# Kernel optimization log

Hardware: AMD Instinct MI355X
Metric: run time of the kernel (lower is better)

## Reference

```python
import jax, jax.numpy as jnp
import numpy as np

# Model dims (match init_kwargs)
E = 16            # real experts
Z = 16            # zero experts (identity)
TOP_K = 4
H = 1024          # hidden_size
I = 512           # intermediate_size per expert
T = 4096          # tokens
ROUTED_SCALING = 1.0


def setup_inputs() -> dict:
    key = jax.random.key(0)
    ks = jax.random.split(key, 6)
    s_h = 1.0 / np.sqrt(H)
    s_i = 1.0 / np.sqrt(I)
    return {
        "hidden_states": jax.random.normal(ks[0], (T, H), jnp.float32),
        # router over E + Z total slots (real experts + zero experts)
        "router_weight": jax.random.normal(ks[1], (E + Z, H), jnp.float32) * s_h,
        "e_score_bias": jax.random.normal(ks[2], (E + Z,), jnp.float32) * 0.01,
        # SwiGLU expert weights
        "w_gate": jax.random.normal(ks[3], (E, H, I), jnp.float32) * s_h,
        "w_up": jax.random.normal(ks[4], (E, H, I), jnp.float32) * s_h,
        "w_down": jax.random.normal(ks[5], (E, I, H), jnp.float32) * s_i,
    }


def reference(hidden_states, router_weight, e_score_bias, w_gate, w_up, w_down):
    x = hidden_states  # [T, H]
    # --- Router (float32, router_dtype == 'float32') ---
    logits = jnp.einsum("th,eh->te", x.astype(jnp.float32), router_weight)  # [T, E+Z]
    scores = jax.nn.softmax(logits, axis=-1)
    # top-k selected on bias-corrected scores; weights taken from raw scores,
    # renormalize=False
    _, topk_ids = jax.lax.top_k(scores + e_score_bias[None, :], TOP_K)  # [T, k]
    topk_w = jnp.take_along_axis(scores, topk_ids, axis=-1)             # [T, k]
    # --- Dispatch/combine weights over all E+Z slots ---
    onehot = jax.nn.one_hot(topk_ids, E + Z, dtype=jnp.float32)  # [T, k, E+Z]
    combine = jnp.einsum("tk,tks->ts", topk_w, onehot)           # [T, E+Z]
    cw_real = combine[:, :E].astype(x.dtype)      # [T, E] routed-expert weights
    zero_w = combine[:, E:].sum(-1).astype(x.dtype)  # [T] identity weight sum
    # --- Grouped-expert SwiGLU (dense dispatch reference) ---
    g = jnp.einsum("th,ehi->eti", x, w_gate)   # [E, T, I]
    u = jnp.einsum("th,ehi->eti", x, w_up)     # [E, T, I]
    act = jax.nn.silu(g) * u
    eout = jnp.einsum("eti,eih->eth", act, w_down)  # [E, T, H]
    routed = jnp.einsum("eth,te->th", eout, cw_real)  # [T, H]
    # zero experts: identity contribution (zero_expert_type == 'identity')
    out = routed * ROUTED_SCALING + zero_w[:, None] * x
    return out
```

## Files before the change

kernel.cpp:

```cpp
#include <hip/hip_runtime.h>
#include <stdint.h>

#define T_TOK 4096
#define Hd    1024
#define Id    512
#define NE    16
#define NSLOT 32
#define TOPK  4
#define CAPR  (T_TOK*TOPK)
#define MAXTILES 144

typedef __bf16 bf16x8 __attribute__((ext_vector_type(8)));
typedef float  floatx4 __attribute__((ext_vector_type(4)));

#define WAIT_VM(n) asm volatile("s_waitcnt vmcnt(" #n ")" ::: "memory")

static __device__ __forceinline__ void wg_barrier(){
  asm volatile("" ::: "memory");
  __builtin_amdgcn_s_barrier();
  asm volatile("" ::: "memory");
}

static __device__ __forceinline__ unsigned short f2bf(float f){
  unsigned int u = __float_as_uint(f);
  u = u + 0x7fffu + ((u >> 16) & 1u);
  return (unsigned short)(u >> 16);
}

static __device__ __forceinline__ void load_lds16(const void* g, void* l){
  __builtin_amdgcn_global_load_lds((const __attribute__((address_space(1))) void*)g,
                                   (__attribute__((address_space(3))) void*)l, 16, 0, 0);
}

__global__ __launch_bounds__(256) void cvt_x_kernel(const float* __restrict__ x,
                                                    unsigned short* __restrict__ xb){
  int i = blockIdx.x * 256 + threadIdx.x;
  float4 v = ((const float4*)x)[i];
  ushort4 o;
  o.x = f2bf(v.x); o.y = f2bf(v.y); o.z = f2bf(v.z); o.w = f2bf(v.w);
  ((ushort4*)xb)[i] = o;
}

__global__ __launch_bounds__(256) void transpose_cvt_kernel(
    const float* __restrict__ src, unsigned short* __restrict__ dst, int R, int C){
  __shared__ float tile[64][65];
  const int e = blockIdx.z;
  const int c0 = blockIdx.x * 64;
  const int r0 = blockIdx.y * 64;
  const float* s = src + (size_t)e * R * C;
  unsigned short* d = dst + (size_t)e * R * C;
  const int lr = threadIdx.x >> 4;
  const int lc = (threadIdx.x & 15) * 4;
  #pragma unroll
  for (int p = 0; p < 4; ++p){
    int r = p*16 + lr;
    float4 v = *(const float4*)(s + (size_t)(r0 + r)*C + c0 + lc);
    tile[r][lc+0] = v.x; tile[r][lc+1] = v.y; tile[r][lc+2] = v.z; tile[r][lc+3] = v.w;
  }
  __syncthreads();
  #pragma unroll
  for (int p = 0; p < 4; ++p){
    int c = p*16 + lr;
    ushort4 o;
    o.x = f2bf(tile[lc+0][c]); o.y = f2bf(tile[lc+1][c]);
    o.z = f2bf(tile[lc+2][c]); o.w = f2bf(tile[lc+3][c]);
    *(ushort4*)(d + (size_t)(c0 + c)*R + r0 + lc) = o;
  }
}

__global__ __launch_bounds__(256) void logits_kernel(const float* __restrict__ x,
    const float* __restrict__ rw, float* __restrict__ logits){
  __shared__ float srw[NSLOT][260];
  const int kc = blockIdx.y * 256;
  const int tid = threadIdx.x;
  #pragma unroll
  for (int p = 0; p < 8; ++p){
    int idx = tid + p*256;
    int s = idx >> 6;
    int c = (idx & 63) << 2;
    float4 v = *(const float4*)(rw + (size_t)s*Hd + kc + c);
    *(float4*)&srw[s][c] = v;
  }
  __syncthreads();
  const int tg = tid >> 3;
  const int sg = tid & 7;
  const int t0 = blockIdx.x * 128 + tg * 4;
  const int s0 = sg * 4;
  float acc[4][4] = {};
  for (int k = 0; k < 256; k += 4){
    float4 r0 = *(const float4*)&srw[s0+0][k];
    float4 r1 = *(const float4*)&srw[s0+1][k];
    float4 r2 = *(const float4*)&srw[s0+2][k];
    float4 r3 = *(const float4*)&srw[s0+3][k];
    #pragma unroll
    for (int tt = 0; tt < 4; ++tt){
      float4 xv = *(const float4*)(x + (size_t)(t0+tt)*Hd + kc + k);
      acc[tt][0] += xv.x*r0.x + xv.y*r0.y + xv.z*r0.z + xv.w*r0.w;
      acc[tt][1] += xv.x*r1.x + xv.y*r1.y + xv.z*r1.z + xv.w*r1.w;
      acc[tt][2] += xv.x*r2.x + xv.y*r2.y + xv.z*r2.z + xv.w*r2.w;
      acc[tt][3] += xv.x*r3.x + xv.y*r3.y + xv.z*r3.z + xv.w*r3.w;
    }
  }
  #pragma unroll
  for (int tt = 0; tt < 4; ++tt)
    #pragma unroll
    for (int s = 0; s < 4; ++s)
      atomicAdd(&logits[(size_t)(t0+tt)*NSLOT + s0 + s], acc[tt][s]);
}

__global__ __launch_bounds__(256) void topk_kernel(
    const float* __restrict__ logits, const float* __restrict__ bias,
    int* __restrict__ counts, int* __restrict__ tkid, float* __restrict__ tkw,
    float* __restrict__ zero_w){
  int t = blockIdx.x * 256 + threadIdx.x;
  float sc[32], bsc[32];
  #pragma unroll
  for (int i = 0; i < 32; i += 4){
    float4 v = *(const float4*)(logits + (size_t)t*NSLOT + i);
    sc[i] = v.x; sc[i+1] = v.y; sc[i+2] = v.z; sc[i+3] = v.w;
  }
  float mx = sc[0];
  #pragma unroll
  for (int i = 1; i < 32; ++i) mx = fmaxf(mx, sc[i]);
  float sum = 0.f;
  #pragma unroll
  for (int i = 0; i < 32; ++i){ sc[i] = __expf(sc[i]-mx); sum += sc[i]; }
  float inv = 1.f / sum;
  #pragma unroll
  for (int i = 0; i < 32; ++i){ sc[i] *= inv; bsc[i] = sc[i] + bias[i]; }
  unsigned int chosen = 0;
  float zw = 0.f;
  #pragma unroll
  for (int k = 0; k < TOPK; ++k){
    float bv = -1e30f, bw = 0.f; int best = 0;
    #pragma unroll
    for (int i = 0; i < 32; ++i){
      float v = ((chosen >> i) & 1u) ? -1e30f : bsc[i];
      if (v > bv){ bv = v; best = i; bw = sc[i]; }
    }
    chosen |= (1u << best);
    tkid[t*TOPK + k] = best;
    tkw[t*TOPK + k]  = bw;
    if (best < NE) atomicAdd(&counts[best], 1);
    else zw += bw;
  }
  zero_w[t] = zw;
}

__global__ void offsets_kernel(const int* __restrict__ counts,
                               int* __restrict__ offsets, int* __restrict__ cursors,
                               int* __restrict__ tilelist, int* __restrict__ ntiles){
  if (threadIdx.x == 0){
    int acc = 0;
    for (int e = 0; e < NE; ++e){ offsets[e] = acc; acc += counts[e]; }
    offsets[NE] = acc;
    int n = 0;
    for (int e = 0; e < NE; ++e){
      int ne = counts[e];
      for (int m = 0; m*128 < ne; ++m) tilelist[n++] = (e << 16) | m;
    }
    ntiles[0] = n;
  }
  if (threadIdx.x < NE) cursors[threadIdx.x] = 0;
}

__global__ __launch_bounds__(256) void build_kernel(
    const int* __restrict__ tkid, const float* __restrict__ tkw,
    const int* __restrict__ offsets, int* __restrict__ cursors,
    int* __restrict__ rowmap, float* __restrict__ roww){
  int i = blockIdx.x * 256 + threadIdx.x;
  int id = tkid[i];
  if (id < NE){
    int pos = atomicAdd(&cursors[id], 1);
    int row = offsets[id] + pos;
    rowmap[row] = i >> 2;
    roww[row]   = tkw[i];
  }
}

__global__ __launch_bounds__(256) void outinit_kernel(const float* __restrict__ x,
    const float* __restrict__ zw, float* __restrict__ out){
  int i = blockIdx.x * 256 + threadIdx.x;
  float s = zw[i >> 8];
  float4 v = ((const float4*)x)[i];
  float4 o; o.x = v.x*s; o.y = v.y*s; o.z = v.z*s; o.w = v.w*s;
  ((float4*)out)[i] = o;
}

__global__ __launch_bounds__(256, 2) void gateup_kernel(
    const unsigned short* __restrict__ xb,
    const unsigned short* __restrict__ wgb,
    const unsigned short* __restrict__ wub,
    const int* __restrict__ offsets,
    const int* __restrict__ rowmap,
    const float* __restrict__ roww,
    const int* __restrict__ tilelist,
    const int* __restrict__ ntiles,
    unsigned short* __restrict__ act){
  const int b = blockIdx.x;
  const int tile = b >> 2;
  if (tile >= ntiles[0]) return;
  const int packed = tilelist[tile];
  const int e  = packed >> 16;
  const int m0 = (packed & 0xffff) * 128;
  const int n0 = (b & 3) * 128;
  const int off = offsets[e];
  const int ne  = offsets[e+1] - off;

  __shared__ unsigned short sA [2][128*32];
  __shared__ unsigned short sBg[2][128*32];
  __shared__ unsigned short sBu[2][128*32];
  __shared__ int sT[128];

  const int tid  = threadIdx.x;
  const int lane = tid & 63;
  const int wid  = tid >> 6;

  if (tid < 128){
    int r = m0 + tid;
    sT[tid] = rowmap[off + ((r < ne) ? r : 0)];
  }
  __syncthreads();

  const int r_in = lane >> 2;
  const int seg  = lane & 3;
  const int rt0  = wid*32 + r_in;
  const int rt1  = rt0 + 16;
  const size_t wbase = (size_t)e * Id * Hd;

  const unsigned short* pA0 = xb + (size_t)sT[rt0]*Hd + seg*8;
  const unsigned short* pA1 = xb + (size_t)sT[rt1]*Hd + seg*8;
  const unsigned short* pG0 = wgb + wbase + (size_t)(n0+rt0)*Hd + seg*8;
  const unsigned short* pG1 = wgb + wbase + (size_t)(n0+rt1)*Hd + seg*8;
  const unsigned short* pU0 = wub + wbase + (size_t)(n0+rt0)*Hd + seg*8;
  const unsigned short* pU1 = wub + wbase + (size_t)(n0+rt1)*Hd + seg*8;
  const int dA0 = wid*1024;
  const int dA1 = wid*1024 + 512;

  floatx4 accg[4][4], accu[4][4];
  #pragma unroll
  for (int i = 0; i < 4; ++i)
    #pragma unroll
    for (int j = 0; j < 4; ++j){
      floatx4 z = {0.f,0.f,0.f,0.f};
      accg[i][j] = z; accu[i][j] = z;
    }

  const int wm = (wid & 1) * 64;
  const int wn = (wid >> 1) * 64;
  const int fm = lane & 15;
  const int fq = lane >> 4;

  load_lds16(pA0, &sA[0][dA0]);  load_lds16(pA1, &sA[0][dA1]);
  load_lds16(pG0, &sBg[0][dA0]); load_lds16(pG1, &sBg[0][dA1]);
  load_lds16(pU0, &sBu[0][dA0]); load_lds16(pU1, &sBu[0][dA1]);

  #pragma unroll 2
  for (int kit = 0; kit < 32; ++kit){
    const int cur = kit & 1;
    if (kit < 31){
      const int nk = (kit+1)*32;
      const int nb = 1 - cur;
      load_lds16(pA0 + nk, &sA[nb][dA0]);  load_lds16(pA1 + nk, &sA[nb][dA1]);
      load_lds16(pG0 + nk, &sBg[nb][dA0]); load_lds16(pG1 + nk, &sBg[nb][dA1]);
      load_lds16(pU0 + nk, &sBu[nb][dA0]); load_lds16(pU1 + nk, &sBu[nb][dA1]);
      WAIT_VM(6);
    } else {
      WAIT_VM(0);
    }
    wg_barrier();
    bf16x8 av[4], bgv[4], buv[4];
    #pragma unroll
    for (int i = 0; i < 4; ++i)
      av[i] = *(const bf16x8*)(&sA[cur][(wm + i*16 + fm)*32 + fq*8]);
    #pragma unroll
    for (int j = 0; j < 4; ++j){
      bgv[j] = *(const bf16x8*)(&sBg[cur][(wn + j*16 + fm)*32 + fq*8]);
      buv[j] = *(const bf16x8*)(&sBu[cur][(wn + j*16 + fm)*32 + fq*8]);
    }
    #pragma unroll
    for (int i = 0; i < 4; ++i)
      #pragma unroll
      for (int j = 0; j < 4; ++j){
        accg[i][j] = __builtin_amdgcn_mfma_f32_16x16x32_bf16(av[i], bgv[j], accg[i][j], 0, 0, 0);
        accu[i][j] = __builtin_amdgcn_mfma_f32_16x16x32_bf16(av[i], buv[j], accu[i][j], 0, 0, 0);
      }
    wg_barrier();
  }

  #pragma unroll
  for (int i = 0; i < 4; ++i){
    #pragma unroll
    for (int r = 0; r < 4; ++r){
      int row = wm + i*16 + fq*4 + r;
      if (m0 + row < ne){
        float w = roww[off + m0 + row];
        size_t rb = (size_t)(off + m0 + row) * Id + n0;
        #pragma unroll
        for (int j = 0; j < 4; ++j){
          float g = accg[i][j][r];
          float u = accu[i][j][r];
          float a = (g / (1.f + __expf(-g))) * u * w;
          act[rb + wn + j*16 + fm] = f2bf(a);
        }
      }
    }
  }
}

__global__ __launch_bounds__(256, 2) void down_kernel(
    const unsigned short* __restrict__ act,
    const unsigned short* __restrict__ wdb,
    const int* __restrict__ offsets,
    const int* __restrict__ rowmap,
    const int* __restrict__ tilelist,
    const int* __restrict__ ntiles,
    float* __restrict__ out){
  const int b = blockIdx.x;
  const int tile = b >> 3;
  if (tile >= ntiles[0]) return;
  const int packed = tilelist[tile];
  const int e  = packed >> 16;
  const int m0 = (packed & 0xffff) * 128;
  const int n0 = (b & 7) * 128;
  const int off = offsets[e];
  const int ne  = offsets[e+1] - off;

  __shared__ unsigned short sA[2][128*32];
  __shared__ unsigned short sB[2][128*32];
  __shared__ int sT[128];

  const int tid  = threadIdx.x;
  const int lane = tid & 63;
  const int wid  = tid >> 6;
  if (tid < 128){
    int r = m0 + tid;
    sT[tid] = (r < ne) ? rowmap[off + r] : 0;
  }

  const int r_in = lane >> 2, seg = lane & 3;
  const int rt0 = wid*32 + r_in;
  const int rt1 = rt0 + 16;
  const int gr0 = off + ((m0 + rt0 < ne) ? (m0 + rt0) : 0);
  const int gr1 = off + ((m0 + rt1 < ne) ? (m0 + rt1) : 0);
  const size_t wbase = (size_t)e * Hd * Id;
  const unsigned short* pA0 = act + (size_t)gr0*Id + seg*8;
  const unsigned short* pA1 = act + (size_t)gr1*Id + seg*8;
  const unsigned short* pB0 = wdb + wbase + (size_t)(n0+rt0)*Id + seg*8;
  const unsigned short* pB1 = wdb + wbase + (size_t)(n0+rt1)*Id + seg*8;
  const int dA0 = wid*1024, dA1 = wid*1024 + 512;

  floatx4 acc[4][4];
  #pragma unroll
  for (int i = 0; i < 4; ++i)
    #pragma unroll
    for (int j = 0; j < 4; ++j){ floatx4 z = {0.f,0.f,0.f,0.f}; acc[i][j] = z; }

  const int wm = (wid & 1) * 64, wn = (wid >> 1) * 64;
  const int fm = lane & 15, fq = lane >> 4;

  load_lds16(pA0, &sA[0][dA0]); load_lds16(pA1, &sA[0][dA1]);
  load_lds16(pB0, &sB[0][dA0]); load_lds16(pB1, &sB[0][dA1]);

  #pragma unroll 2
  for (int kit = 0; kit < 16; ++kit){
    const int cur = kit & 1;
    if (kit < 15){
      const int nk = (kit+1)*32;
      const int nb = 1 - cur;
      load_lds16(pA0 + nk, &sA[nb][dA0]); load_lds16(pA1 + nk, &sA[nb][dA1]);
      load_lds16(pB0 + nk, &sB[nb][dA0]); load_lds16(pB1 + nk, &sB[nb][dA1]);
      WAIT_VM(4);
    } else {
      WAIT_VM(0);
    }
    wg_barrier();
    bf16x8 av[4], bv[4];
    #pragma unroll
    for (int i = 0; i < 4; ++i) av[i] = *(const bf16x8*)(&sA[cur][(wm + i*16 + fm)*32 + fq*8]);
    #pragma unroll
    for (int j = 0; j < 4; ++j) bv[j] = *(const bf16x8*)(&sB[cur][(wn + j*16 + fm)*32 + fq*8]);
    #pragma unroll
    for (int i = 0; i < 4; ++i)
      #pragma unroll
      for (int j = 0; j < 4; ++j)
        acc[i][j] = __builtin_amdgcn_mfma_f32_16x16x32_bf16(av[i], bv[j], acc[i][j], 0, 0, 0);
    wg_barrier();
  }

  #pragma unroll
  for (int i = 0; i < 4; ++i){
    #pragma unroll
    for (int r = 0; r < 4; ++r){
      int row = wm + i*16 + fq*4 + r;
      if (m0 + row < ne){
        int t = sT[row];
        #pragma unroll
        for (int j = 0; j < 4; ++j)
          atomicAdd(&out[(size_t)t*Hd + n0 + wn + j*16 + fm], acc[i][j][r]);
      }
    }
  }
}

extern "C" void kernel_launch(void* const* d_in, const int* in_sizes, int n_in,
                              void* d_out, int out_size, void* d_ws, size_t ws_size,
                              hipStream_t stream){
  (void)in_sizes; (void)n_in; (void)out_size; (void)ws_size;
  const float* x    = (const float*)d_in[0];
  const float* rw   = (const float*)d_in[1];
  const float* bias = (const float*)d_in[2];
  const float* wg   = (const float*)d_in[3];
  const float* wu   = (const float*)d_in[4];
  const float* wd   = (const float*)d_in[5];
  float* out = (float*)d_out;

  char* ws = (char*)d_ws;
  const size_t WSZ = (size_t)NE * Id * Hd * 2;
  unsigned short* wgb = (unsigned short*)(ws);
  unsigned short* wub = (unsigned short*)(ws + WSZ);
  unsigned short* wdb = (unsigned short*)(ws + 2*WSZ);
  unsigned short* xb  = (unsigned short*)(ws + 3*WSZ);
  unsigned short* act = (unsigned short*)(ws + 3*WSZ + (size_t)T_TOK*Hd*2);
  char* misc = ws + 3*WSZ + (size_t)T_TOK*Hd*2 + (size_t)CAPR*Id*2;

  const size_t LOGB = (size_t)T_TOK * NSLOT * 4;
  float* logits = (float*)misc;
  int*   counts  = (int*)(misc + LOGB);
  int*   cursors = counts + 16;
  int*   offsets = cursors + 16;
  char* p2 = misc + LOGB + 256;
  int*   tkid   = (int*)p2;                         p2 += (size_t)T_TOK*TOPK*4;
  float* tkw    = (float*)p2;                       p2 += (size_t)T_TOK*TOPK*4;
  float* zerow  = (float*)p2;                       p2 += (size_t)T_TOK*4;
  int*   rowmap = (int*)p2;                         p2 += (size_t)CAPR*4;
  float* roww   = (float*)p2;                       p2 += (size_t)CAPR*4;
  int*   tilelist = (int*)p2;                       p2 += (size_t)MAXTILES*4;
  int*   ntiles   = (int*)p2;

  hipMemsetAsync(misc, 0, LOGB + 256, stream);

  cvt_x_kernel<<<T_TOK*Hd/4/256, 256, 0, stream>>>(x, xb);
  transpose_cvt_kernel<<<dim3(Id/64, Hd/64, NE), 256, 0, stream>>>(wg, wgb, Hd, Id);
  transpose_cvt_kernel<<<dim3(Id/64, Hd/64, NE), 256, 0, stream>>>(wu, wub, Hd, Id);
  transpose_cvt_kernel<<<dim3(Hd/64, Id/64, NE), 256, 0, stream>>>(wd, wdb, Id, Hd);

  logits_kernel<<<dim3(T_TOK/128, Hd/256), 256, 0, stream>>>(x, rw, logits);
  topk_kernel<<<T_TOK/256, 256, 0, stream>>>(logits, bias, counts, tkid, tkw, zerow);
  offsets_kernel<<<1, 64, 0, stream>>>(counts, offsets, cursors, tilelist, ntiles);
  build_kernel<<<CAPR/256, 256, 0, stream>>>(tkid, tkw, offsets, cursors, rowmap, roww);

  outinit_kernel<<<T_TOK*Hd/4/256, 256, 0, stream>>>(x, zerow, out);

  gateup_kernel<<<MAXTILES*4, 256, 0, stream>>>(
      xb, wgb, wub, offsets, rowmap, roww, tilelist, ntiles, act);
  down_kernel<<<MAXTILES*8, 256, 0, stream>>>(
      act, wdb, offsets, rowmap, tilelist, ntiles, out);
}
```

Before: 319.8 us.

## Merge prep kernels, drop memset and atomics, fuse zero-expert init into top-k

```diff
diff --git a/kernel.cpp b/kernel.cpp
--- a/kernel.cpp
+++ b/kernel.cpp
@@ -32,87 +32,98 @@
                                    (__attribute__((address_space(3))) void*)l, 16, 0, 0);
 }
 
-__global__ __launch_bounds__(256) void cvt_x_kernel(const float* __restrict__ x,
-                                                    unsigned short* __restrict__ xb){
-  int i = blockIdx.x * 256 + threadIdx.x;
-  float4 v = ((const float4*)x)[i];
-  ushort4 o;
-  o.x = f2bf(v.x); o.y = f2bf(v.y); o.z = f2bf(v.z); o.w = f2bf(v.w);
-  ((ushort4*)xb)[i] = o;
-}
-
-__global__ __launch_bounds__(256) void transpose_cvt_kernel(
-    const float* __restrict__ src, unsigned short* __restrict__ dst, int R, int C){
+__global__ __launch_bounds__(256) void prep_kernel(
+    const float* __restrict__ wg, const float* __restrict__ wu,
+    const float* __restrict__ wd, const float* __restrict__ x,
+    unsigned short* __restrict__ wgb, unsigned short* __restrict__ wub,
+    unsigned short* __restrict__ wdb, unsigned short* __restrict__ xb){
   __shared__ float tile[64][65];
-  const int e = blockIdx.z;
-  const int c0 = blockIdx.x * 64;
-  const int r0 = blockIdx.y * 64;
-  const float* s = src + (size_t)e * R * C;
-  unsigned short* d = dst + (size_t)e * R * C;
-  const int lr = threadIdx.x >> 4;
-  const int lc = (threadIdx.x & 15) * 4;
-  #pragma unroll
-  for (int p = 0; p < 4; ++p){
-    int r = p*16 + lr;
-    float4 v = *(const float4*)(s + (size_t)(r0 + r)*C + c0 + lc);
-    tile[r][lc+0] = v.x; tile[r][lc+1] = v.y; tile[r][lc+2] = v.z; tile[r][lc+3] = v.w;
-  }
-  __syncthreads();
-  #pragma unroll
-  for (int p = 0; p < 4; ++p){
-    int c = p*16 + lr;
-    ushort4 o;
-    o.x = f2bf(tile[lc+0][c]); o.y = f2bf(tile[lc+1][c]);
-    o.z = f2bf(tile[lc+2][c]); o.w = f2bf(tile[lc+3][c]);
-    *(ushort4*)(d + (size_t)(c0 + c)*R + r0 + lc) = o;
+  const int bid = blockIdx.x;
+  const int tid = threadIdx.x;
+  if (bid < 6144){
+    const float* src; unsigned short* dst; int R, C, cx, ry;
+    const int arr = bid >> 11;
+    const int rem = bid & 2047;
+    const int e = rem >> 7;
+    const int r2 = rem & 127;
+    if (arr == 0){ src = wg; dst = wgb; R = Hd; C = Id; cx = r2 & 7;  ry = r2 >> 3; }
+    else if (arr == 1){ src = wu; dst = wub; R = Hd; C = Id; cx = r2 & 7;  ry = r2 >> 3; }
+    else { src = wd; dst = wdb; R = Id; C = Hd; cx = r2 & 15; ry = r2 >> 4; }
+    const int c0 = cx * 64, r0 = ry * 64;
+    const float* s = src + (size_t)e * R * C;
+    unsigned short* d = dst + (size_t)e * R * C;
+    const int lr = tid >> 4;
+    const int lc = (tid & 15) * 4;
+    #pragma unroll
+    for (int p = 0; p < 4; ++p){
+      int r = p*16 + lr;
+      float4 v = *(const float4*)(s + (size_t)(r0 + r)*C + c0 + lc);
+      tile[r][lc+0] = v.x; tile[r][lc+1] = v.y; tile[r][lc+2] = v.z; tile[r][lc+3] = v.w;
+    }
+    __syncthreads();
+    #pragma unroll
+    for (int p = 0; p < 4; ++p){
+      int c = p*16 + lr;
+      ushort4 o;
+      o.x = f2bf(tile[lc+0][c]); o.y = f2bf(tile[lc+1][c]);
+      o.z = f2bf(tile[lc+2][c]); o.w = f2bf(tile[lc+3][c]);
+      *(ushort4*)(d + (size_t)(c0 + c)*R + r0 + lc) = o;
+    }
+  } else {
+    const int ib = (bid - 6144) * 1024;
+    #pragma unroll
+    for (int p = 0; p < 4; ++p){
+      int i = ib + p*256 + tid;
+      float4 v = ((const float4*)x)[i];
+      ushort4 o;
+      o.x = f2bf(v.x); o.y = f2bf(v.y); o.z = f2bf(v.z); o.w = f2bf(v.w);
+      ((ushort4*)xb)[i] = o;
+    }
   }
 }
 
 __global__ __launch_bounds__(256) void logits_kernel(const float* __restrict__ x,
-    const float* __restrict__ rw, float* __restrict__ logits){
+    const float* __restrict__ rw, float* __restrict__ logits, int* __restrict__ counts){
+  if (blockIdx.x == 0 && threadIdx.x < NE) counts[threadIdx.x] = 0;
   __shared__ float srw[NSLOT][260];
-  const int kc = blockIdx.y * 256;
   const int tid = threadIdx.x;
-  #pragma unroll
-  for (int p = 0; p < 8; ++p){
-    int idx = tid + p*256;
-    int s = idx >> 6;
-    int c = (idx & 63) << 2;
-    float4 v = *(const float4*)(rw + (size_t)s*Hd + kc + c);
-    *(float4*)&srw[s][c] = v;
-  }
-  __syncthreads();
-  const int tg = tid >> 3;
-  const int sg = tid & 7;
-  const int t0 = blockIdx.x * 128 + tg * 4;
-  const int s0 = sg * 4;
-  float acc[4][4] = {};
-  for (int k = 0; k < 256; k += 4){
-    float4 r0 = *(const float4*)&srw[s0+0][k];
-    float4 r1 = *(const float4*)&srw[s0+1][k];
-    float4 r2 = *(const float4*)&srw[s0+2][k];
-    float4 r3 = *(const float4*)&srw[s0+3][k];
-    #pragma unroll
-    for (int tt = 0; tt < 4; ++tt){
-      float4 xv = *(const float4*)(x + (size_t)(t0+tt)*Hd + kc + k);
-      acc[tt][0] += xv.x*r0.x + xv.y*r0.y + xv.z*r0.z + xv.w*r0.w;
-      acc[tt][1] += xv.x*r1.x + xv.y*r1.y + xv.z*r1.z + xv.w*r1.w;
-      acc[tt][2] += xv.x*r2.x + xv.y*r2.y + xv.z*r2.z + xv.w*r2.w;
-      acc[tt][3] += xv.x*r3.x + xv.y*r3.y + xv.z*r3.z + xv.w*r3.w;
-    }
-  }
-  #pragma unroll
-  for (int tt = 0; tt < 4; ++tt)
-    #pragma unroll
-    for (int s = 0; s < 4; ++s)
-      atomicAdd(&logits[(size_t)(t0+tt)*NSLOT + s0 + s], acc[tt][s]);
+  const int t  = blockIdx.x * 32 + (tid >> 3);
+  const int s0 = (tid & 7) * 4;
+  float4 acc = {0.f, 0.f, 0.f, 0.f};
+  for (int c = 0; c < 4; ++c){
+    const int kc = c * 256;
+    __syncthreads();
+    #pragma unroll
+    for (int p = 0; p < 8; ++p){
+      int idx = tid + p*256;
+      int s = idx >> 6;
+      int col = (idx & 63) << 2;
+      *(float4*)&srw[s][col] = *(const float4*)(rw + (size_t)s*Hd + kc + col);
+    }
+    __syncthreads();
+    for (int k = 0; k < 256; k += 4){
+      float4 xv = *(const float4*)(x + (size_t)t*Hd + kc + k);
+      float4 r0 = *(const float4*)&srw[s0+0][k];
+      float4 r1 = *(const float4*)&srw[s0+1][k];
+      float4 r2 = *(const float4*)&srw[s0+2][k];
+      float4 r3 = *(const float4*)&srw[s0+3][k];
+      acc.x += xv.x*r0.x + xv.y*r0.y + xv.z*r0.z + xv.w*r0.w;
+      acc.y += xv.x*r1.x + xv.y*r1.y + xv.z*r1.z + xv.w*r1.w;
+      acc.z += xv.x*r2.x + xv.y*r2.y + xv.z*r2.z + xv.w*r2.w;
+      acc.w += xv.x*r3.x + xv.y*r3.y + xv.z*r3.z + xv.w*r3.w;
+    }
+  }
+  *(float4*)(logits + (size_t)t*NSLOT + s0) = acc;
 }
 
 __global__ __launch_bounds__(256) void topk_kernel(
     const float* __restrict__ logits, const float* __restrict__ bias,
+    const float* __restrict__ x,
     int* __restrict__ counts, int* __restrict__ tkid, float* __restrict__ tkw,
-    float* __restrict__ zero_w){
-  int t = blockIdx.x * 256 + threadIdx.x;
+    float* __restrict__ out){
+  __shared__ float szw[256];
+  const int tid = threadIdx.x;
+  const int t = blockIdx.x * 256 + tid;
   float sc[32], bsc[32];
   #pragma unroll
   for (int i = 0; i < 32; i += 4){
@@ -144,7 +155,21 @@
     if (best < NE) atomicAdd(&counts[best], 1);
     else zw += bw;
   }
-  zero_w[t] = zw;
+  szw[tid] = zw;
+  __syncthreads();
+  const int lane = tid & 63, wid = tid >> 6;
+  const size_t base = (size_t)blockIdx.x * 256 * Hd;
+  for (int r = wid; r < 256; r += 4){
+    float s = szw[r];
+    const float4* xs = (const float4*)(x + base + (size_t)r*Hd);
+    float4* os = (float4*)(out + base + (size_t)r*Hd);
+    #pragma unroll
+    for (int q = 0; q < 4; ++q){
+      float4 v = xs[lane + q*64];
+      float4 o; o.x = v.x*s; o.y = v.y*s; o.z = v.z*s; o.w = v.w*s;
+      os[lane + q*64] = o;
+    }
+  }
 }
 
 __global__ void offsets_kernel(const int* __restrict__ counts,
@@ -178,16 +203,7 @@
   }
 }
 
-__global__ __launch_bounds__(256) void outinit_kernel(const float* __restrict__ x,
-    const float* __restrict__ zw, float* __restrict__ out){
-  int i = blockIdx.x * 256 + threadIdx.x;
-  float s = zw[i >> 8];
-  float4 v = ((const float4*)x)[i];
-  float4 o; o.x = v.x*s; o.y = v.y*s; o.z = v.z*s; o.w = v.w*s;
-  ((float4*)out)[i] = o;
-}
-
-__global__ __launch_bounds__(256, 2) void gateup_kernel(
+__global__ __launch_bounds__(256, 3) void gateup_kernel(
     const unsigned short* __restrict__ xb,
     const unsigned short* __restrict__ wgb,
     const unsigned short* __restrict__ wub,
@@ -308,7 +324,7 @@
   }
 }
 
-__global__ __launch_bounds__(256, 2) void down_kernel(
+__global__ __launch_bounds__(256, 4) void down_kernel(
     const unsigned short* __restrict__ act,
     const unsigned short* __restrict__ wdb,
     const int* __restrict__ offsets,
@@ -432,26 +448,16 @@
   char* p2 = misc + LOGB + 256;
   int*   tkid   = (int*)p2;                         p2 += (size_t)T_TOK*TOPK*4;
   float* tkw    = (float*)p2;                       p2 += (size_t)T_TOK*TOPK*4;
-  float* zerow  = (float*)p2;                       p2 += (size_t)T_TOK*4;
   int*   rowmap = (int*)p2;                         p2 += (size_t)CAPR*4;
   float* roww   = (float*)p2;                       p2 += (size_t)CAPR*4;
   int*   tilelist = (int*)p2;                       p2 += (size_t)MAXTILES*4;
   int*   ntiles   = (int*)p2;
 
-  hipMemsetAsync(misc, 0, LOGB + 256, stream);
-
-  cvt_x_kernel<<<T_TOK*Hd/4/256, 256, 0, stream>>>(x, xb);
-  transpose_cvt_kernel<<<dim3(Id/64, Hd/64, NE), 256, 0, stream>>>(wg, wgb, Hd, Id);
-  transpose_cvt_kernel<<<dim3(Id/64, Hd/64, NE), 256, 0, stream>>>(wu, wub, Hd, Id);
-  transpose_cvt_kernel<<<dim3(Hd/64, Id/64, NE), 256, 0, stream>>>(wd, wdb, Id, Hd);
-
-  logits_kernel<<<dim3(T_TOK/128, Hd/256), 256, 0, stream>>>(x, rw, logits);
-  topk_kernel<<<T_TOK/256, 256, 0, stream>>>(logits, bias, counts, tkid, tkw, zerow);
+  prep_kernel<<<7168, 256, 0, stream>>>(wg, wu, wd, x, wgb, wub, wdb, xb);
+  logits_kernel<<<T_TOK/32, 256, 0, stream>>>(x, rw, logits, counts);
+  topk_kernel<<<T_TOK/256, 256, 0, stream>>>(logits, bias, x, counts, tkid, tkw, out);
   offsets_kernel<<<1, 64, 0, stream>>>(counts, offsets, cursors, tilelist, ntiles);
   build_kernel<<<CAPR/256, 256, 0, stream>>>(tkid, tkw, offsets, cursors, rowmap, roww);
-
-  outinit_kernel<<<T_TOK*Hd/4/256, 256, 0, stream>>>(x, zerow, out);
-
   gateup_kernel<<<MAXTILES*4, 256, 0, stream>>>(
       xb, wgb, wub, offsets, rowmap, roww, tilelist, ntiles, act);
   down_kernel<<<MAXTILES*8, 256, 0, stream>>>(
```

New measurement: 513.0 us. +60.4%, slower.
